# Performance work log

Measured on AMD Instinct MI355X. Metric: run time of the kernel, lower is better.

Reference implementation:

```python
import jax, jax.numpy as jnp
import numpy as np

H = 64          # hidden_size
NG = 5000       # num_genes
B = 32          # num_graphs
N = B * NG      # total nodes
E = 1_600_000   # total edges


def setup_inputs() -> dict:
    key = jax.random.key(0)
    ks = jax.random.split(key, 32)
    def nrm(k, shape, s=0.05):
        return jax.random.normal(k, shape, jnp.float32) * s
    return {
        "x": jax.random.normal(ks[0], (N, 2), jnp.float32),
        "edge_index": jax.random.randint(ks[1], (2, E), 0, N),
        # pert_w: Linear(1, H); gene_basal_w: Linear(1, H)
        "pert_w_W": nrm(ks[2], (H, 1)), "pert_w_b": nrm(ks[3], (H,)),
        "basal_W": nrm(ks[4], (H, 1)), "basal_b": nrm(ks[5], (H,)),
        # gene embedding table (max_norm=True -> rows renormed to norm<=1)
        "emb_table": nrm(ks[6], (NG, H), 0.5),
        # emb_trans: Linear(2H, H)
        "emb_trans_W": nrm(ks[7], (H, 2 * H)), "emb_trans_b": nrm(ks[8], (H,)),
        # pert_base_trans_w: Linear(2H, H)  (gene_pert_agg == 'concat+w')
        "pbt_W": nrm(ks[9], (H, 2 * H)), "pbt_b": nrm(ks[10], (H,)),
        # two GCNConv(H, H) layers
        "gcn1_W": nrm(ks[11], (H, H)), "gcn1_b": nrm(ks[12], (H,)),
        "gcn2_W": nrm(ks[13], (H, H)), "gcn2_b": nrm(ks[14], (H,)),
        # recovery_w: MLP([H, 2H, H, 1]) with BN on first two hidden layers
        "rec_W1": nrm(ks[15], (2 * H, H)), "rec_b1": nrm(ks[16], (2 * H,)),
        "rec_g1": jnp.ones((2 * H,), jnp.float32), "rec_be1": jnp.zeros((2 * H,), jnp.float32),
        "rec_W2": nrm(ks[17], (H, 2 * H)), "rec_b2": nrm(ks[18], (H,)),
        "rec_g2": jnp.ones((H,), jnp.float32), "rec_be2": jnp.zeros((H,), jnp.float32),
        "rec_W3": nrm(ks[19], (1, H)), "rec_b3": nrm(ks[20], (1,)),
    }


def _gcn_conv(h, src, dst, norm, W, b, n_nodes):
    # PyG GCNConv: x' = scatter_add(norm * (x W^T)[src] -> dst) + b, self-loops included in src/dst
    m = h @ W.T                                   # [N, H]
    out = jax.ops.segment_sum(m[src] * norm[:, None], dst, num_segments=n_nodes)
    return out + b


def _batchnorm(z, g, b, eps=1e-5):
    mu = z.mean(0)
    var = z.var(0)
    return (z - mu) * jax.lax.rsqrt(var + eps) * g + b


def reference(x, edge_index, pert_w_W, pert_w_b, basal_W, basal_b, emb_table,
              emb_trans_W, emb_trans_b, pbt_W, pbt_b, gcn1_W, gcn1_b,
              gcn2_W, gcn2_b, rec_W1, rec_b1, rec_g1, rec_be1,
              rec_W2, rec_b2, rec_g2, rec_be2, rec_W3, rec_b3):
    n_nodes = x.shape[0]
    ng = emb_table.shape[0]
    nb = n_nodes // ng

    # GCN normalization with self-loops (computed once, shared by both layers)
    loop = jnp.arange(n_nodes)
    src = jnp.concatenate([edge_index[0], loop])
    dst = jnp.concatenate([edge_index[1], loop])
    deg = jax.ops.segment_sum(jnp.ones_like(src, jnp.float32), dst, num_segments=n_nodes)
    dinv = jnp.where(deg > 0, jax.lax.rsqrt(jnp.maximum(deg, 1.0)), 0.0)
    norm = dinv[src] * dinv[dst]

    pert_emb = x[:, 1:2] @ pert_w_W.T + pert_w_b          # [N, H]
    base = x[:, 0:1] @ basal_W.T + basal_b                # [N, H]

    # nn.Embedding(max_norm=True): renorm rows to max L2 norm of 1
    nrm = jnp.linalg.norm(emb_table, axis=1, keepdims=True)
    emb_n = emb_table * jnp.minimum(1.0, 1.0 / jnp.maximum(nrm, 1e-7))
    emb = jnp.tile(emb_n, (nb, 1))                        # arange(NG).repeat(B) lookup
    base_emb = jnp.concatenate([emb, base], axis=1) @ emb_trans_W.T + emb_trans_b

    def pbt(p, b_):
        return jnp.concatenate([p, b_], axis=1) @ pbt_W.T + pbt_b

    h = pbt(pert_emb, base_emb)
    h = pbt(jax.nn.relu(_gcn_conv(h, src, dst, norm, gcn1_W, gcn1_b, n_nodes)), base_emb)
    h = pbt(jax.nn.relu(_gcn_conv(h, src, dst, norm, gcn2_W, gcn2_b, n_nodes)), base_emb)

    # recovery_w: Linear -> BN -> ReLU -> Linear -> BN -> ReLU -> Linear
    z = jax.nn.relu(_batchnorm(h @ rec_W1.T + rec_b1, rec_g1, rec_be1))
    z = jax.nn.relu(_batchnorm(z @ rec_W2.T + rec_b2, rec_g2, rec_be2))
    out = z @ rec_W3.T + rec_b3                           # [N, 1]
    return out.reshape(nb, ng)
```

## Files before the change

### kernel.cpp

```cpp
#include <hip/hip_runtime.h>


#define GS_GRID 2048
#define GS_BLK  256

enum { A1_=0, A0_=64, C1_=128, C0_=192, D1_=256, D0_=320,
       S1_=384, Q1_=512, SC1_=640, SH1_=768,
       S2_=896, Q2_=960, SC2_=1024, SH2_=1088,
       GD1_=1152, GA1_=1216, G00_=1280,
       GD2_=1344, G02_=1408, RD1_=1472, RD0_=1600, CST_FLOATS=2048 };

__device__ __forceinline__ float wave_sum64(float v) {
#pragma unroll
  for (int o = 32; o; o >>= 1) v += __shfl_xor(v, o, 64);
  return v;
}

__device__ __forceinline__ int rfl(int v) { return __builtin_amdgcn_readfirstlane(v); }

__device__ __forceinline__ float rlane(float v, int k) {
  return __int_as_float(__builtin_amdgcn_readlane(__float_as_int(v), k));
}

__global__ __launch_bounds__(256) void hist_k(const int* __restrict__ ei,
                                              int* __restrict__ hist, int E) {
  __shared__ int h[256];
  const int t = threadIdx.x;
  h[t] = 0;
  __syncthreads();
  const int per = (E + gridDim.x - 1) / gridDim.x;
  const int beg = blockIdx.x * per, end = min(E, beg + per);
  for (int i = beg + t; i < end; i += 256)
    atomicAdd(&h[ei[E + i] >> 10], 1);
  __syncthreads();
  hist[blockIdx.x * 256 + t] = h[t];
}

__global__ void scan1b_k(int* __restrict__ hist, int* __restrict__ bsum) {
  __shared__ int sc[256];
  const int t = threadIdx.x;
  const int b = blockIdx.x;
  int v = hist[t * 256 + b];
  sc[t] = v; __syncthreads();
  for (int o = 1; o < 256; o <<= 1) {
    int x = sc[t]; if (t >= o) x += sc[t - o];
    __syncthreads(); sc[t] = x; __syncthreads();
  }
  hist[t * 256 + b] = sc[t] - v;
  if (t == 255) bsum[b] = sc[t];
}

__global__ void scan2b_k(const int* __restrict__ bsum, int* __restrict__ bucketBase,
                         int* __restrict__ rowptrN, int E) {
  __shared__ int sc[256];
  const int t = threadIdx.x;
  int v = bsum[t];
  sc[t] = v; __syncthreads();
  for (int o = 1; o < 256; o <<= 1) {
    int x = sc[t]; if (t >= o) x += sc[t - o];
    __syncthreads(); sc[t] = x; __syncthreads();
  }
  bucketBase[t] = sc[t] - v;
  if (t == 255) { bucketBase[256] = sc[t]; rowptrN[0] = E; }
}

__global__ __launch_bounds__(256) void bucket_k(const int* __restrict__ ei,
                                                const int* __restrict__ hist,
                                                const int* __restrict__ bucketBase,
                                                int2* __restrict__ eb, int E) {
  __shared__ int cur[256];
  const int t = threadIdx.x;
  cur[t] = hist[blockIdx.x * 256 + t] + bucketBase[t];
  __syncthreads();
  const int per = (E + gridDim.x - 1) / gridDim.x;
  const int beg = blockIdx.x * per, end = min(E, beg + per);
  for (int i = beg + t; i < end; i += 256) {
    int s = ei[i], d = ei[E + i];
    int pos = atomicAdd(&cur[d >> 10], 1);
    eb[pos] = make_int2(s, d);
  }
}

__global__ __launch_bounds__(256) void csr_k(const int2* __restrict__ eb,
                                             const int* __restrict__ bucketBase,
                                             int* __restrict__ rowptr, float* __restrict__ dinv,
                                             int* __restrict__ col, int N) {
  __shared__ int cnt[1024];
  __shared__ int base[1024];
  __shared__ int red[256];
  const int t = threadIdx.x;
  const int k = blockIdx.x;
  const int nodeBeg = k << 10;
  const int segBeg = bucketBase[k], segEnd = bucketBase[k + 1];
#pragma unroll
  for (int j = t; j < 1024; j += 256) cnt[j] = 0;
  __syncthreads();
  for (int i = segBeg + t; i < segEnd; i += 256)
    atomicAdd(&cnt[eb[i].y & 1023], 1);
  __syncthreads();
  int c0 = cnt[4 * t], c1 = cnt[4 * t + 1], c2 = cnt[4 * t + 2], c3 = cnt[4 * t + 3];
  int ts = c0 + c1 + c2 + c3;
  red[t] = ts; __syncthreads();
  for (int o = 1; o < 256; o <<= 1) {
    int x = red[t]; if (t >= o) x += red[t - o];
    __syncthreads(); red[t] = x; __syncthreads();
  }
  int off = red[t] - ts;
  base[4 * t] = off;
  base[4 * t + 1] = off + c0;
  base[4 * t + 2] = off + c0 + c1;
  base[4 * t + 3] = off + c0 + c1 + c2;
#pragma unroll
  for (int u = 0; u < 4; ++u) {
    int j = 4 * t + u;
    int node = nodeBeg + j;
    if (node < N) {
      rowptr[node] = segBeg + base[j];
      dinv[node] = rsqrtf((float)(cnt[j] + 1));
    }
  }
  __syncthreads();
  cnt[4 * t] = base[4 * t]; cnt[4 * t + 1] = base[4 * t + 1];
  cnt[4 * t + 2] = base[4 * t + 2]; cnt[4 * t + 3] = base[4 * t + 3];
  __syncthreads();
  for (int i = segBeg + t; i < segEnd; i += 256) {
    int2 e = eb[i];
    int pos = atomicAdd(&cnt[e.y & 1023], 1);
    col[segBeg + pos] = e.x;
  }
}

__global__ void consts1_k(const float* __restrict__ pbtW, const float* __restrict__ pertW,
                          const float* __restrict__ pertB, const float* __restrict__ etW,
                          const float* __restrict__ basW, const float* __restrict__ basB,
                          const float* __restrict__ etB, float* __restrict__ cst) {
  int h = threadIdx.x;
  float a1 = 0, a0 = 0, c1 = 0, c0 = 0;
  for (int k = 0; k < 64; ++k) {
    float wp = pbtW[h * 128 + k];
    a1 = fmaf(wp, pertW[k], a1);
    a0 = fmaf(wp, pertB[k], a0);
    float we = etW[h * 128 + 64 + k];
    c1 = fmaf(we, basW[k], c1);
    c0 = fmaf(we, basB[k], c0);
  }
  cst[A1_ + h] = a1; cst[A0_ + h] = a0; cst[C1_ + h] = c1; cst[C0_ + h] = c0 + etB[h];
}

__global__ void consts2_k(const float* __restrict__ pbtW, const float* __restrict__ pbtB,
                          float* __restrict__ cst) {
  int h = threadIdx.x;
  float d1 = 0, d0 = 0;
  for (int k = 0; k < 64; ++k) {
    float w = pbtW[h * 128 + 64 + k];
    d1 = fmaf(w, cst[C1_ + k], d1);
    d0 = fmaf(w, cst[C0_ + k], d0);
  }
  cst[D1_ + h] = d1; cst[D0_ + h] = d0 + pbtB[h];
}

__global__ void consts3_k(const float* __restrict__ g1W, float* __restrict__ cst) {
  int h = threadIdx.x;
  float gd1 = 0, ga1 = 0, g00 = 0;
  for (int k = 0; k < 64; ++k) {
    float w = g1W[h * 64 + k];
    gd1 = fmaf(w, cst[D1_ + k], gd1);
    ga1 = fmaf(w, cst[A1_ + k], ga1);
    g00 = fmaf(w, cst[D0_ + k] + cst[A0_ + k], g00);
  }
  cst[GD1_ + h] = gd1; cst[GA1_ + h] = ga1; cst[G00_ + h] = g00;
}

__global__ void consts5_k(const float* __restrict__ g2W, float* __restrict__ cst) {
  int h = threadIdx.x;
  float a = 0, b = 0;
  for (int k = 0; k < 64; ++k) {
    float w = g2W[h * 64 + k];
    a = fmaf(w, cst[D1_ + k], a);
    b = fmaf(w, cst[D0_ + k], b);
  }
  cst[GD2_ + h] = a; cst[G02_ + h] = b;
}

__global__ void consts6_k(const float* __restrict__ rW1, const float* __restrict__ rb1,
                          float* __restrict__ cst) {
  int c = threadIdx.x;
  float a = 0, b = 0;
  for (int k = 0; k < 64; ++k) {
    float w = rW1[c * 64 + k];
    a = fmaf(w, cst[D1_ + k], a);
    b = fmaf(w, cst[D0_ + k], b);
  }
  cst[RD1_ + c] = a; cst[RD0_ + c] = b + rb1[c];
}

__global__ void constsW_k(const float* __restrict__ g2W, const float* __restrict__ rW1,
                          const float* __restrict__ pbtW,
                          float* __restrict__ Wf, float* __restrict__ Wr) {
  const int t = threadIdx.x;
  for (int e = t; e < 4096; e += 256) {
    int c = e >> 6, j = e & 63;
    float s = 0.f;
    for (int h = 0; h < 64; ++h) s = fmaf(g2W[c * 64 + h], pbtW[h * 128 + j], s);
    Wf[e] = s;
  }
  for (int e = t; e < 8192; e += 256) {
    int c = e >> 6, j = e & 63;
    float s = 0.f;
    for (int h = 0; h < 64; ++h) s = fmaf(rW1[c * 64 + h], pbtW[h * 128 + j], s);
    Wr[e] = s;
  }
}

template <bool NORM>
__global__ __launch_bounds__(256) void geneT_k(const float* __restrict__ in,
                                               const float* __restrict__ W, int ldw,
                                               float* __restrict__ out, int NG) {
  const int lane = threadIdx.x & 63;
  const int wid = blockIdx.x * 4 + (threadIdx.x >> 6);
  const int nw = gridDim.x * 4;
  float w[64];
#pragma unroll
  for (int j = 0; j < 16; ++j) {
    float4 v = *reinterpret_cast<const float4*>(W + lane * ldw + 4 * j);
    w[4 * j] = v.x; w[4 * j + 1] = v.y; w[4 * j + 2] = v.z; w[4 * j + 3] = v.w;
  }
  for (int g = wid; g < NG; g += nw) {
    float e = in[g * 64 + lane];
    if (NORM) {
      float sq = wave_sum64(e * e);
      float nrm = sqrtf(sq);
      float s = nrm > 1.f ? 1.f / nrm : 1.f;
      e *= s;
    }
    float acc = 0.f;
#pragma unroll
    for (int k = 0; k < 64; ++k) acc = fmaf(w[k], rlane(e, k), acc);
    out[g * 64 + lane] = acc;
  }
}

__global__ __launch_bounds__(256) void m1_k(const float* __restrict__ x,
                                            const float* __restrict__ embTm1,
                                            const float* __restrict__ dinv,
                                            const float* __restrict__ cst,
                                            float* __restrict__ m1, int N, int NG) {
  int total = N * 16;
  for (int idx = blockIdx.x * blockDim.x + threadIdx.x; idx < total;
       idx += gridDim.x * blockDim.x) {
    int n = idx >> 4, q = idx & 15;
    int g = n % NG;
    float x0 = x[2 * n], x1 = x[2 * n + 1], dn = dinv[n];
    float4 em = *reinterpret_cast<const float4*>(embTm1 + g * 64 + q * 4);
    float4 gd1 = *reinterpret_cast<const float4*>(cst + GD1_ + q * 4);
    float4 ga1 = *reinterpret_cast<const float4*>(cst + GA1_ + q * 4);
    float4 g00 = *reinterpret_cast<const float4*>(cst + G00_ + q * 4);
    float4 mv;
    mv.x = dn * (fmaf(x0, gd1.x, fmaf(x1, ga1.x, em.x + g00.x)));
    mv.y = dn * (fmaf(x0, gd1.y, fmaf(x1, ga1.y, em.y + g00.y)));
    mv.z = dn * (fmaf(x0, gd1.z, fmaf(x1, ga1.z, em.z + g00.z)));
    mv.w = dn * (fmaf(x0, gd1.w, fmaf(x1, ga1.w, em.w + g00.w)));
    reinterpret_cast<float4*>(m1)[idx] = mv;
  }
}

#define XS_STRIDE 130
#define WS_STRIDE 68
#define OS_STRIDE 68
#define OS_WORDS  (128 * OS_STRIDE)
#define WS_WORDS  (64 * WS_STRIDE)
#define LDS_WORDS (OS_WORDS + WS_WORDS + 128)

__device__ __forceinline__ int osslot(int f, int row) { return (f + 2 * row) % 17; }
__device__ __forceinline__ int xswz(int k) { return 2 * ((k >> 2) & 7); }

__device__ __forceinline__ void stage_xsw(const float* __restrict__ in, int ldin,
                                          int inOff, int base, int N, float* Xs, int t) {
#pragma unroll
  for (int c = 0; c < 8; ++c) {
    int lin = c * 256 + t;
    int nl = lin >> 4, k4 = lin & 15;
    int row = base + nl; if (row >= N) row = N - 1;
    float4 v = *reinterpret_cast<const float4*>(in + (size_t)row * ldin + inOff + 4 * k4);
    const int csw = nl ^ (2 * (k4 & 7));
    Xs[(4 * k4 + 0) * XS_STRIDE + csw] = v.x;
    Xs[(4 * k4 + 1) * XS_STRIDE + csw] = v.y;
    Xs[(4 * k4 + 2) * XS_STRIDE + csw] = v.z;
    Xs[(4 * k4 + 3) * XS_STRIDE + csw] = v.w;
  }
}

template <bool MUL_D>
__global__ __launch_bounds__(256, 4) void gemmt_gv_k(
    const float* __restrict__ in,
    const float* __restrict__ W,
    const float* __restrict__ tbl,
    const float* __restrict__ cA, const float* __restrict__ cB,
    const float* __restrict__ x, const float* __restrict__ dinv,
    float* __restrict__ out, int ldout, int N, int NG) {
  __shared__ float lds[LDS_WORDS];
  float* Xs = lds;
  float* Ws = lds + OS_WORDS;
  const int t = threadIdx.x;
  const int base = blockIdx.x << 7;

#pragma unroll
  for (int c = 0; c < 16; ++c) {
    int lin = c * 256 + t;
    int cw = lin >> 6, kw = lin & 63;
    Ws[kw * WS_STRIDE + cw] = W[cw * 64 + kw];
  }
  stage_xsw(in, 64, 0, base, N, Xs, t);
  __syncthreads();

  const int ng = t & 31;
  const int c0 = (t >> 5) * 8;
  float acc[8][4];
#pragma unroll
  for (int i = 0; i < 8; ++i)
#pragma unroll
    for (int j = 0; j < 4; ++j) acc[i][j] = 0.f;
#pragma unroll 4
  for (int k = 0; k < 64; ++k) {
    float4 wa = *reinterpret_cast<const float4*>(Ws + k * WS_STRIDE + c0);
    float4 wb = *reinterpret_cast<const float4*>(Ws + k * WS_STRIDE + c0 + 4);
    const int cb = (2 * ng) ^ xswz(k);
    float2 xa = *reinterpret_cast<const float2*>(Xs + k * XS_STRIDE + cb);
    float2 xb = *reinterpret_cast<const float2*>(Xs + k * XS_STRIDE + cb + 64);
    const float w8[8] = {wa.x, wa.y, wa.z, wa.w, wb.x, wb.y, wb.z, wb.w};
    const float x4[4] = {xa.x, xa.y, xb.x, xb.y};
#pragma unroll
    for (int ci = 0; ci < 8; ++ci)
#pragma unroll
      for (int xi = 0; xi < 4; ++xi)
        acc[ci][xi] = fmaf(w8[ci], x4[xi], acc[ci][xi]);
  }
  __syncthreads();

  const int nd[4] = {2 * ng, 2 * ng + 1, 2 * ng + 64, 2 * ng + 65};
  const int f0 = c0 >> 2;
#pragma unroll
  for (int xi = 0; xi < 4; ++xi) {
    const int r = nd[xi];
    float4 p0 = make_float4(acc[0][xi], acc[1][xi], acc[2][xi], acc[3][xi]);
    float4 p1 = make_float4(acc[4][xi], acc[5][xi], acc[6][xi], acc[7][xi]);
    *reinterpret_cast<float4*>(Xs + r * OS_STRIDE + 4 * osslot(f0, r)) = p0;
    *reinterpret_cast<float4*>(Xs + r * OS_STRIDE + 4 * osslot(f0 + 1, r)) = p1;
  }
  __syncthreads();

  const int q = t & 15;
  const float4 a4 = *reinterpret_cast<const float4*>(cA + 4 * q);
  const float4 b4 = *reinterpret_cast<const float4*>(cB + 4 * q);
#pragma unroll
  for (int c = 0; c < 8; ++c) {
    int nl = c * 16 + (t >> 4);
    int n = base + nl;
    if (n < N) {
      float4 o = *reinterpret_cast<const float4*>(Xs + nl * OS_STRIDE + 4 * osslot(q, nl));
      int g = n % NG;
      float4 tg = *reinterpret_cast<const float4*>(tbl + (size_t)g * 64 + 4 * q);
      float x0 = x[2 * n];
      o.x += fmaf(x0, a4.x, tg.x + b4.x);
      o.y += fmaf(x0, a4.y, tg.y + b4.y);
      o.z += fmaf(x0, a4.z, tg.z + b4.z);
      o.w += fmaf(x0, a4.w, tg.w + b4.w);
      if (MUL_D) {
        float dv = dinv[n];
        o.x *= dv; o.y *= dv; o.z *= dv; o.w *= dv;
      }
      *reinterpret_cast<float4*>(out + (size_t)n * ldout + 4 * q) = o;
    }
  }
}

__global__ __launch_bounds__(256, 4) void gemmt_rec1_k(
    const float* __restrict__ in,
    const float* __restrict__ Wr,
    const float* __restrict__ tblA, const float* __restrict__ tblB,
    const float* __restrict__ cA, const float* __restrict__ cB,
    const float* __restrict__ x,
    float* __restrict__ Z,
    float* __restrict__ sums, float* __restrict__ sqs, int N, int NG) {
  __shared__ float lds[LDS_WORDS];
  float* Xs = lds;
  float* Ws = lds + OS_WORDS;
  float* sred = lds + OS_WORDS + WS_WORDS;
  const int t = threadIdx.x;
  const int base = blockIdx.x << 7;
  if (t < 128) sred[t] = 0.f;

#pragma unroll
  for (int c = 0; c < 16; ++c) {
    int lin = c * 256 + t;
    int cw = lin >> 6, kw = lin & 63;
    Ws[kw * WS_STRIDE + cw] = Wr[cw * 64 + kw];
  }
  stage_xsw(in, 64, 0, base, N, Xs, t);
  __syncthreads();

  const int ng = t & 31;
  const int c0 = (t >> 5) * 8;
  float accA[8][4], accB[8][4];
#pragma unroll
  for (int i = 0; i < 8; ++i)
#pragma unroll
    for (int j = 0; j < 4; ++j) { accA[i][j] = 0.f; accB[i][j] = 0.f; }

#pragma unroll 4
  for (int k = 0; k < 64; ++k) {
    float4 wa = *reinterpret_cast<const float4*>(Ws + k * WS_STRIDE + c0);
    float4 wb = *reinterpret_cast<const float4*>(Ws + k * WS_STRIDE + c0 + 4);
    const int cb = (2 * ng) ^ xswz(k);
    float2 xa = *reinterpret_cast<const float2*>(Xs + k * XS_STRIDE + cb);
    float2 xb = *reinterpret_cast<const float2*>(Xs + k * XS_STRIDE + cb + 64);
    const float w8[8] = {wa.x, wa.y, wa.z, wa.w, wb.x, wb.y, wb.z, wb.w};
    const float x4[4] = {xa.x, xa.y, xb.x, xb.y};
#pragma unroll
    for (int ci = 0; ci < 8; ++ci)
#pragma unroll
      for (int xi = 0; xi < 4; ++xi)
        accA[ci][xi] = fmaf(w8[ci], x4[xi], accA[ci][xi]);
  }
  __syncthreads();
#pragma unroll
  for (int c = 0; c < 16; ++c) {
    int lin = c * 256 + t;
    int cw = lin >> 6, kw = lin & 63;
    Ws[kw * WS_STRIDE + cw] = Wr[(64 + cw) * 64 + kw];
  }
  __syncthreads();
#pragma unroll 4
  for (int k = 0; k < 64; ++k) {
    float4 wa = *reinterpret_cast<const float4*>(Ws + k * WS_STRIDE + c0);
    float4 wb = *reinterpret_cast<const float4*>(Ws + k * WS_STRIDE + c0 + 4);
    const int cb = (2 * ng) ^ xswz(k);
    float2 xa = *reinterpret_cast<const float2*>(Xs + k * XS_STRIDE + cb);
    float2 xb = *reinterpret_cast<const float2*>(Xs + k * XS_STRIDE + cb + 64);
    const float w8[8] = {wa.x, wa.y, wa.z, wa.w, wb.x, wb.y, wb.z, wb.w};
    const float x4[4] = {xa.x, xa.y, xb.x, xb.y};
#pragma unroll
    for (int ci = 0; ci < 8; ++ci)
#pragma unroll
      for (int xi = 0; xi < 4; ++xi)
        accB[ci][xi] = fmaf(w8[ci], x4[xi], accB[ci][xi]);
  }
  __syncthreads();

  const int nd[4] = {2 * ng, 2 * ng + 1, 2 * ng + 64, 2 * ng + 65};
  const int f0 = c0 >> 2;
  const int q = t & 15;

#pragma unroll
  for (int xi = 0; xi < 4; ++xi) {
    const int r = nd[xi];
    float4 p0 = make_float4(accA[0][xi], accA[1][xi], accA[2][xi], accA[3][xi]);
    float4 p1 = make_float4(accA[4][xi], accA[5][xi], accA[6][xi], accA[7][xi]);
    *reinterpret_cast<float4*>(Xs + r * OS_STRIDE + 4 * osslot(f0, r)) = p0;
    *reinterpret_cast<float4*>(Xs + r * OS_STRIDE + 4 * osslot(f0 + 1, r)) = p1;
  }
  __syncthreads();
  {
    const float4 a4 = *reinterpret_cast<const float4*>(cA + 4 * q);
    const float4 b4 = *reinterpret_cast<const float4*>(cB + 4 * q);
    float4 s4 = make_float4(0.f, 0.f, 0.f, 0.f);
    float4 q4 = make_float4(0.f, 0.f, 0.f, 0.f);
#pragma unroll
    for (int c = 0; c < 8; ++c) {
      int nl = c * 16 + (t >> 4);
      int n = base + nl;
      if (n < N) {
        float4 o = *reinterpret_cast<const float4*>(Xs + nl * OS_STRIDE + 4 * osslot(q, nl));
        int g = n % NG;
        float4 tg = *reinterpret_cast<const float4*>(tblA + (size_t)g * 64 + 4 * q);
        float x0 = x[2 * n];
        o.x += fmaf(x0, a4.x, tg.x + b4.x);
        o.y += fmaf(x0, a4.y, tg.y + b4.y);
        o.z += fmaf(x0, a4.z, tg.z + b4.z);
        o.w += fmaf(x0, a4.w, tg.w + b4.w);
        *reinterpret_cast<float4*>(Z + (size_t)n * 128 + 4 * q) = o;
        s4.x += o.x; s4.y += o.y; s4.z += o.z; s4.w += o.w;
        q4.x += o.x * o.x; q4.y += o.y * o.y; q4.z += o.z * o.z; q4.w += o.w * o.w;
      }
    }
    atomicAdd(&sred[4 * q + 0], s4.x); atomicAdd(&sred[4 * q + 1], s4.y);
    atomicAdd(&sred[4 * q + 2], s4.z); atomicAdd(&sred[4 * q + 3], s4.w);
    atomicAdd(&sred[64 + 4 * q + 0], q4.x); atomicAdd(&sred[64 + 4 * q + 1], q4.y);
    atomicAdd(&sred[64 + 4 * q + 2], q4.z); atomicAdd(&sred[64 + 4 * q + 3], q4.w);
  }
  __syncthreads();
  if (t < 64) {
    atomicAdd(&sums[t], sred[t]);
    atomicAdd(&sqs[t], sred[64 + t]);
  }
  __syncthreads();
  if (t < 128) sred[t] = 0.f;
  __syncthreads();

#pragma unroll
  for (int xi = 0; xi < 4; ++xi) {
    const int r = nd[xi];
    float4 p0 = make_float4(accB[0][xi], accB[1][xi], accB[2][xi], accB[3][xi]);
    float4 p1 = make_float4(accB[4][xi], accB[5][xi], accB[6][xi], accB[7][xi]);
    *reinterpret_cast<float4*>(Xs + r * OS_STRIDE + 4 * osslot(f0, r)) = p0;
    *reinterpret_cast<float4*>(Xs + r * OS_STRIDE + 4 * osslot(f0 + 1, r)) = p1;
  }
  __syncthreads();
  {
    const float4 a4 = *reinterpret_cast<const float4*>(cA + 64 + 4 * q);
    const float4 b4 = *reinterpret_cast<const float4*>(cB + 64 + 4 * q);
    float4 s4 = make_float4(0.f, 0.f, 0.f, 0.f);
    float4 q4 = make_float4(0.f, 0.f, 0.f, 0.f);
#pragma unroll
    for (int c = 0; c < 8; ++c) {
      int nl = c * 16 + (t >> 4);
      int n = base + nl;
      if (n < N) {
        float4 o = *reinterpret_cast<const float4*>(Xs + nl * OS_STRIDE + 4 * osslot(q, nl));
        int g = n % NG;
        float4 tg = *reinterpret_cast<const float4*>(tblB + (size_t)g * 64 + 4 * q);
        float x0 = x[2 * n];
        o.x += fmaf(x0, a4.x, tg.x + b4.x);
        o.y += fmaf(x0, a4.y, tg.y + b4.y);
        o.z += fmaf(x0, a4.z, tg.z + b4.z);
        o.w += fmaf(x0, a4.w, tg.w + b4.w);
        *reinterpret_cast<float4*>(Z + (size_t)n * 128 + 64 + 4 * q) = o;
        s4.x += o.x; s4.y += o.y; s4.z += o.z; s4.w += o.w;
        q4.x += o.x * o.x; q4.y += o.y * o.y; q4.z += o.z * o.z; q4.w += o.w * o.w;
      }
    }
    atomicAdd(&sred[4 * q + 0], s4.x); atomicAdd(&sred[4 * q + 1], s4.y);
    atomicAdd(&sred[4 * q + 2], s4.z); atomicAdd(&sred[4 * q + 3], s4.w);
    atomicAdd(&sred[64 + 4 * q + 0], q4.x); atomicAdd(&sred[64 + 4 * q + 1], q4.y);
    atomicAdd(&sred[64 + 4 * q + 2], q4.z); atomicAdd(&sred[64 + 4 * q + 3], q4.w);
  }
  __syncthreads();
  if (t < 64) {
    atomicAdd(&sums[64 + t], sred[t]);
    atomicAdd(&sqs[64 + t], sred[64 + t]);
  }
}

__global__ __launch_bounds__(256, 4) void gemmt_rec2_k(
    const float* __restrict__ Z,
    const float* __restrict__ W,
    const float* __restrict__ b,
    const float* __restrict__ bnsc, const float* __restrict__ bnsh,
    float* __restrict__ out,
    float* __restrict__ sums, float* __restrict__ sqs, int N) {
  __shared__ float lds[LDS_WORDS];
  float* Xs = lds;
  float* Ws = lds + OS_WORDS;
  float* sred = lds + OS_WORDS + WS_WORDS;
  const int t = threadIdx.x;
  const int base = blockIdx.x << 7;
  if (t < 128) sred[t] = 0.f;

  const int ng = t & 31;
  const int c0 = (t >> 5) * 8;
  float acc[8][4];
#pragma unroll
  for (int i = 0; i < 8; ++i)
#pragma unroll
    for (int j = 0; j < 4; ++j) acc[i][j] = 0.f;

  for (int half = 0; half < 2; ++half) {
    if (half) __syncthreads();
    const int ko = half * 64;
#pragma unroll
    for (int c = 0; c < 16; ++c) {
      int lin = c * 256 + t;
      int cw = lin >> 6, kw = lin & 63;
      Ws[kw * WS_STRIDE + cw] = W[cw * 128 + ko + kw];
    }
#pragma unroll
    for (int c = 0; c < 8; ++c) {
      int lin = c * 256 + t;
      int nl = lin >> 4, k4 = lin & 15;
      int row = base + nl; if (row >= N) row = N - 1;
      float4 v = *reinterpret_cast<const float4*>(Z + (size_t)row * 128 + ko + 4 * k4);
      float4 sc = *reinterpret_cast<const float4*>(bnsc + ko + 4 * k4);
      float4 sh = *reinterpret_cast<const float4*>(bnsh + ko + 4 * k4);
      v.x = fmaxf(fmaf(v.x, sc.x, sh.x), 0.f);
      v.y = fmaxf(fmaf(v.y, sc.y, sh.y), 0.f);
      v.z = fmaxf(fmaf(v.z, sc.z, sh.z), 0.f);
      v.w = fmaxf(fmaf(v.w, sc.w, sh.w), 0.f);
      const int csw = nl ^ (2 * (k4 & 7));
      Xs[(4 * k4 + 0) * XS_STRIDE + csw] = v.x;
      Xs[(4 * k4 + 1) * XS_STRIDE + csw] = v.y;
      Xs[(4 * k4 + 2) * XS_STRIDE + csw] = v.z;
      Xs[(4 * k4 + 3) * XS_STRIDE + csw] = v.w;
    }
    __syncthreads();
#pragma unroll 4
    for (int k = 0; k < 64; ++k) {
      float4 wa = *reinterpret_cast<const float4*>(Ws + k * WS_STRIDE + c0);
      float4 wb = *reinterpret_cast<const float4*>(Ws + k * WS_STRIDE + c0 + 4);
      const int cb = (2 * ng) ^ xswz(k);
      float2 xa = *reinterpret_cast<const float2*>(Xs + k * XS_STRIDE + cb);
      float2 xb = *reinterpret_cast<const float2*>(Xs + k * XS_STRIDE + cb + 64);
      const float w8[8] = {wa.x, wa.y, wa.z, wa.w, wb.x, wb.y, wb.z, wb.w};
      const float x4[4] = {xa.x, xa.y, xb.x, xb.y};
#pragma unroll
      for (int ci = 0; ci < 8; ++ci)
#pragma unroll
        for (int xi = 0; xi < 4; ++xi)
          acc[ci][xi] = fmaf(w8[ci], x4[xi], acc[ci][xi]);
    }
  }
  __syncthreads();

  const int nd[4] = {2 * ng, 2 * ng + 1, 2 * ng + 64, 2 * ng + 65};
  const int f0 = c0 >> 2;
#pragma unroll
  for (int xi = 0; xi < 4; ++xi) {
    const int r = nd[xi];
    float4 p0 = make_float4(acc[0][xi], acc[1][xi], acc[2][xi], acc[3][xi]);
    float4 p1 = make_float4(acc[4][xi], acc[5][xi], acc[6][xi], acc[7][xi]);
    *reinterpret_cast<float4*>(Xs + r * OS_STRIDE + 4 * osslot(f0, r)) = p0;
    *reinterpret_cast<float4*>(Xs + r * OS_STRIDE + 4 * osslot(f0 + 1, r)) = p1;
  }
  __syncthreads();

  const int q = t & 15;
  const float4 bb = *reinterpret_cast<const float4*>(b + 4 * q);
  float4 s4 = make_float4(0.f, 0.f, 0.f, 0.f);
  float4 q4 = make_float4(0.f, 0.f, 0.f, 0.f);
#pragma unroll
  for (int c = 0; c < 8; ++c) {
    int nl = c * 16 + (t >> 4);
    int n = base + nl;
    if (n < N) {
      float4 o = *reinterpret_cast<const float4*>(Xs + nl * OS_STRIDE + 4 * osslot(q, nl));
      o.x += bb.x; o.y += bb.y; o.z += bb.z; o.w += bb.w;
      *reinterpret_cast<float4*>(out + (size_t)n * 64 + 4 * q) = o;
      s4.x += o.x; s4.y += o.y; s4.z += o.z; s4.w += o.w;
      q4.x += o.x * o.x; q4.y += o.y * o.y; q4.z += o.z * o.z; q4.w += o.w * o.w;
    }
  }
  atomicAdd(&sred[4 * q + 0], s4.x); atomicAdd(&sred[4 * q + 1], s4.y);
  atomicAdd(&sred[4 * q + 2], s4.z); atomicAdd(&sred[4 * q + 3], s4.w);
  atomicAdd(&sred[64 + 4 * q + 0], q4.x); atomicAdd(&sred[64 + 4 * q + 1], q4.y);
  atomicAdd(&sred[64 + 4 * q + 2], q4.z); atomicAdd(&sred[64 + 4 * q + 3], q4.w);
  __syncthreads();
  if (t < 64) {
    atomicAdd(&sums[t], sred[t]);
    atomicAdd(&sqs[t], sred[64 + t]);
  }
}

__global__ __launch_bounds__(256) void gather_k(const float* __restrict__ m,
                                                const int* __restrict__ rowptr,
                                                const int* __restrict__ col,
                                                const float* __restrict__ dinv,
                                                const float* __restrict__ bias,
                                                float* __restrict__ out, int N) {
  const int lane = threadIdx.x & 63;
  const int wid = blockIdx.x * 4 + (threadIdx.x >> 6);
  const int nw = gridDim.x * 4;
  const float b = bias[lane];
  for (int n = wid; n < N; n += nw) {
    const int nn = rfl(n);
    const float dn = dinv[nn];
    float a0 = m[(size_t)nn * 64 + lane];
    float a1 = 0.f, a2 = 0.f, a3 = 0.f;
    const int beg = rfl(rowptr[nn]), end = rfl(rowptr[nn + 1]);
    for (int base = beg; base < end; base += 64) {
      const int rem = end - base;
      const int kk = rem < 64 ? rem : 64;
      int cv = (lane < kk) ? col[base + lane] : 0;
      int k = 0;
      for (; k + 7 < kk; k += 8) {
        int i0 = __shfl(cv, k, 64),     i1 = __shfl(cv, k + 1, 64);
        int i2 = __shfl(cv, k + 2, 64), i3 = __shfl(cv, k + 3, 64);
        int i4 = __shfl(cv, k + 4, 64), i5 = __shfl(cv, k + 5, 64);
        int i6 = __shfl(cv, k + 6, 64), i7 = __shfl(cv, k + 7, 64);
        float v0 = m[(size_t)i0 * 64 + lane];
        float v1 = m[(size_t)i1 * 64 + lane];
        float v2 = m[(size_t)i2 * 64 + lane];
        float v3 = m[(size_t)i3 * 64 + lane];
        float v4 = m[(size_t)i4 * 64 + lane];
        float v5 = m[(size_t)i5 * 64 + lane];
        float v6 = m[(size_t)i6 * 64 + lane];
        float v7 = m[(size_t)i7 * 64 + lane];
        a0 += v0 + v4; a1 += v1 + v5; a2 += v2 + v6; a3 += v3 + v7;
      }
      for (; k + 1 < kk; k += 2) {
        int i0 = __shfl(cv, k, 64), i1 = __shfl(cv, k + 1, 64);
        float v0 = m[(size_t)i0 * 64 + lane];
        float v1 = m[(size_t)i1 * 64 + lane];
        a0 += v0; a1 += v1;
      }
      if (k < kk) a0 += m[(size_t)__shfl(cv, k, 64) * 64 + lane];
    }
    float acc = (a0 + a1) + (a2 + a3);
    out[(size_t)nn * 64 + lane] = fmaxf(fmaf(dn, acc, b), 0.f);
  }
}

__global__ void bnparam_k(const float* __restrict__ sums, const float* __restrict__ sqs,
                          const float* __restrict__ g, const float* __restrict__ be,
                          float* __restrict__ scale, float* __restrict__ shift, int C,
                          float invN) {
  int t = threadIdx.x;
  if (t < C) {
    float mu = sums[t] * invN;
    float var = fmaxf(sqs[t] * invN - mu * mu, 0.f);
    float sc = g[t] * rsqrtf(var + 1e-5f);
    scale[t] = sc;
    shift[t] = be[t] - mu * sc;
  }
}

__global__ __launch_bounds__(256) void rec3_k(const float* __restrict__ z2,
                                              const float* __restrict__ scale,
                                              const float* __restrict__ shift,
                                              const float* __restrict__ W3,
                                              const float* __restrict__ b3,
                                              float* __restrict__ out, int N) {
  const int lane = threadIdx.x & 63;
  const int wid = blockIdx.x * 4 + (threadIdx.x >> 6);
  const int nw = gridDim.x * 4;
  const float sc = scale[lane], sh = shift[lane], w = W3[lane], b = b3[0];
  for (int n = wid; n < N; n += nw) {
    float v = z2[(size_t)n * 64 + lane];
    v = fmaxf(fmaf(v, sc, sh), 0.f) * w;
    v = wave_sum64(v);
    if (lane == 0) out[n] = v + b;
  }
}

extern "C" void kernel_launch(void* const* d_in, const int* in_sizes, int n_in,
                              void* d_out, int out_size, void* d_ws, size_t ws_size,
                              hipStream_t stream) {
  const float* x     = (const float*)d_in[0];
  const int*   ei    = (const int*)d_in[1];
  const float* pertW = (const float*)d_in[2];
  const float* pertB = (const float*)d_in[3];
  const float* basW  = (const float*)d_in[4];
  const float* basB  = (const float*)d_in[5];
  const float* embTb = (const float*)d_in[6];
  const float* etW   = (const float*)d_in[7];
  const float* etB   = (const float*)d_in[8];
  const float* pbtW  = (const float*)d_in[9];
  const float* pbtB  = (const float*)d_in[10];
  const float* g1W   = (const float*)d_in[11];
  const float* g1B   = (const float*)d_in[12];
  const float* g2W   = (const float*)d_in[13];
  const float* g2B   = (const float*)d_in[14];
  const float* rW1   = (const float*)d_in[15];
  const float* rb1   = (const float*)d_in[16];
  const float* rg1   = (const float*)d_in[17];
  const float* rbe1  = (const float*)d_in[18];
  const float* rW2   = (const float*)d_in[19];
  const float* rb2   = (const float*)d_in[20];
  const float* rg2   = (const float*)d_in[21];
  const float* rbe2  = (const float*)d_in[22];
  const float* rW3   = (const float*)d_in[23];
  const float* rb3   = (const float*)d_in[24];
  float* outp = (float*)d_out;

  const int N  = in_sizes[0] / 2;
  const int E  = in_sizes[1] / 2;
  const int NG = in_sizes[6] / 64;
  const int NB = (N + 1023) >> 10;
  const int NT = (N + 127) >> 7;

  char* p = (char*)d_ws;
  float* cst    = (float*)p; p += CST_FLOATS * 4;
  int*   hist   = (int*)p;   p += 256 * 256 * 4;
  int*   bb     = (int*)p;   p += 1024;
  int*   bsum   = (int*)p;   p += 1024;
  int*   rowptr = (int*)p;   p += (size_t)(N + 64) * 4;
  float* dinv   = (float*)p; p += (size_t)N * 4;
  int*   col    = (int*)p;   p += (size_t)E * 4;
  float* Wf     = (float*)p; p += 4096 * 4;
  float* Wr     = (float*)p; p += 8192 * 4;
  float* embT   = (float*)p; p += (size_t)NG * 64 * 4;
  float* embT2  = (float*)p; p += (size_t)NG * 64 * 4;
  float* embT2g2= (float*)p; p += (size_t)NG * 64 * 4;
  float* embT2rA= (float*)p; p += (size_t)NG * 64 * 4;
  float* embT2rB= (float*)p; p += (size_t)NG * 64 * 4;
  float* z2buf  = (float*)p; p += (size_t)N * 64 * 4;
  float* hb     = (float*)p; p += (size_t)N * 64 * 4;
  float* tmp1   = (float*)p; p += (size_t)N * 64 * 4;
  float* tmp2   = (float*)p; p += (size_t)N * 64 * 4;
  float* Z = hb;
  float* z2 = z2buf;
  float* embTm1 = embT;
  int2*  eb = (int2*)tmp2;

  dim3 blk(GS_BLK), grid(GS_GRID);

  hipMemsetAsync(cst, 0, CST_FLOATS * 4, stream);

  hist_k<<<256, 256, 0, stream>>>(ei, hist, E);
  scan1b_k<<<256, 256, 0, stream>>>(hist, bsum);
  scan2b_k<<<1, 256, 0, stream>>>(bsum, bb, rowptr + N, E);
  bucket_k<<<256, 256, 0, stream>>>(ei, hist, bb, eb, E);
  csr_k<<<NB, 256, 0, stream>>>(eb, bb, rowptr, dinv, col, N);

  consts1_k<<<1, 64, 0, stream>>>(pbtW, pertW, pertB, etW, basW, basB, etB, cst);
  consts2_k<<<1, 64, 0, stream>>>(pbtW, pbtB, cst);
  consts3_k<<<1, 64, 0, stream>>>(g1W, cst);
  consts5_k<<<1, 64, 0, stream>>>(g2W, cst);
  consts6_k<<<1, 128, 0, stream>>>(rW1, rb1, cst);
  constsW_k<<<1, 256, 0, stream>>>(g2W, rW1, pbtW, Wf, Wr);
  geneT_k<true><<<256, 256, 0, stream>>>(embTb, etW, 128, embT, NG);
  geneT_k<false><<<256, 256, 0, stream>>>(embT, pbtW + 64, 128, embT2, NG);
  geneT_k<false><<<256, 256, 0, stream>>>(embT2, g1W, 64, embTm1, NG);
  geneT_k<false><<<256, 256, 0, stream>>>(embT2, g2W, 64, embT2g2, NG);
  geneT_k<false><<<256, 256, 0, stream>>>(embT2, rW1, 64, embT2rA, NG);
  geneT_k<false><<<256, 256, 0, stream>>>(embT2, rW1 + 64 * 64, 64, embT2rB, NG);
  m1_k<<<grid, blk, 0, stream>>>(x, embTm1, dinv, cst, tmp1, N, NG);

  gather_k<<<grid, blk, 0, stream>>>(tmp1, rowptr, col, dinv, g1B, tmp2, N);
  gemmt_gv_k<true><<<NT, blk, 0, stream>>>(
      tmp2, Wf, embT2g2, cst + GD2_, cst + G02_, x, dinv, tmp1, 64, N, NG);
  gather_k<<<grid, blk, 0, stream>>>(tmp1, rowptr, col, dinv, g2B, tmp2, N);

  gemmt_rec1_k<<<NT, blk, 0, stream>>>(
      tmp2, Wr, embT2rA, embT2rB, cst + RD1_, cst + RD0_, x, Z,
      cst + S1_, cst + Q1_, N, NG);
  bnparam_k<<<1, 128, 0, stream>>>(cst + S1_, cst + Q1_, rg1, rbe1,
                                   cst + SC1_, cst + SH1_, 128, 1.0f / (float)N);
  gemmt_rec2_k<<<NT, blk, 0, stream>>>(Z, rW2, rb2, cst + SC1_, cst + SH1_,
                                       z2, cst + S2_, cst + Q2_, N);
  bnparam_k<<<1, 64, 0, stream>>>(cst + S2_, cst + Q2_, rg2, rbe2,
                                  cst + SC2_, cst + SH2_, 64, 1.0f / (float)N);
  rec3_k<<<grid, blk, 0, stream>>>(z2, cst + SC2_, cst + SH2_, rW3, rb3, outp, N);
}
```

Baseline: 489.0 us.

## Fuse first-layer message construction into the gather via compact node records

Instead of materializing the full N×64 first-layer message tensor and then gathering it, a small per-node record (x0, x1, dinv, gene id) is written and the gather recomputes each neighbor's message on the fly from the gene embedding table and the constants. This removes a large write and a large scattered read of 64-float rows, replacing them with 16-byte record reads plus reads from a small, cache-resident 5000×64 table. The cost is more per-edge arithmetic and a dependent load chain (record, then table) per neighbor. The gather also applies bias and relu, matching what the old gather did.

After: 489.0 us. No clear change (-0.0%).

```diff
diff --git a/kernel.cpp b/kernel.cpp
--- a/kernel.cpp
+++ b/kernel.cpp
@@ -240,27 +240,62 @@
   }
 }
 
-__global__ __launch_bounds__(256) void m1_k(const float* __restrict__ x,
-                                            const float* __restrict__ embTm1,
-                                            const float* __restrict__ dinv,
-                                            const float* __restrict__ cst,
-                                            float* __restrict__ m1, int N, int NG) {
-  int total = N * 16;
-  for (int idx = blockIdx.x * blockDim.x + threadIdx.x; idx < total;
-       idx += gridDim.x * blockDim.x) {
-    int n = idx >> 4, q = idx & 15;
+__global__ __launch_bounds__(256) void nrec_k(const float* __restrict__ x,
+                                              const float* __restrict__ dinv,
+                                              float4* __restrict__ nrec, int N, int NG) {
+  for (int n = blockIdx.x * blockDim.x + threadIdx.x; n < N; n += gridDim.x * blockDim.x) {
     int g = n % NG;
-    float x0 = x[2 * n], x1 = x[2 * n + 1], dn = dinv[n];
-    float4 em = *reinterpret_cast<const float4*>(embTm1 + g * 64 + q * 4);
-    float4 gd1 = *reinterpret_cast<const float4*>(cst + GD1_ + q * 4);
-    float4 ga1 = *reinterpret_cast<const float4*>(cst + GA1_ + q * 4);
-    float4 g00 = *reinterpret_cast<const float4*>(cst + G00_ + q * 4);
-    float4 mv;
-    mv.x = dn * (fmaf(x0, gd1.x, fmaf(x1, ga1.x, em.x + g00.x)));
-    mv.y = dn * (fmaf(x0, gd1.y, fmaf(x1, ga1.y, em.y + g00.y)));
-    mv.z = dn * (fmaf(x0, gd1.z, fmaf(x1, ga1.z, em.z + g00.z)));
-    mv.w = dn * (fmaf(x0, gd1.w, fmaf(x1, ga1.w, em.w + g00.w)));
-    reinterpret_cast<float4*>(m1)[idx] = mv;
+    nrec[n] = make_float4(x[2 * n], x[2 * n + 1], dinv[n], __int_as_float(g));
+  }
+}
+
+__global__ __launch_bounds__(256) void gather1_k(
+    const float4* __restrict__ nrec, const float* __restrict__ embTm1,
+    const int* __restrict__ rowptr, const int* __restrict__ col,
+    const float* __restrict__ dinv, const float* __restrict__ cst,
+    const float* __restrict__ bias, float* __restrict__ out, int N) {
+  const int lane = threadIdx.x & 63;
+  const int wid = blockIdx.x * 4 + (threadIdx.x >> 6);
+  const int nw = gridDim.x * 4;
+  const float gd1 = cst[GD1_ + lane];
+  const float ga1 = cst[GA1_ + lane];
+  const float g00 = cst[G00_ + lane];
+  const float b = bias[lane];
+  for (int n = wid; n < N; n += nw) {
+    const int nn = rfl(n);
+    const float dn = dinv[nn];
+    float4 r0 = nrec[nn];
+    float e0 = embTm1[(size_t)__float_as_int(r0.w) * 64 + lane];
+    float a0 = r0.z * fmaf(r0.x, gd1, fmaf(r0.y, ga1, e0 + g00));
+    float a1 = 0.f, a2 = 0.f, a3 = 0.f;
+    const int beg = rfl(rowptr[nn]), end = rfl(rowptr[nn + 1]);
+    for (int base = beg; base < end; base += 64) {
+      const int rem = end - base;
+      const int kk = rem < 64 ? rem : 64;
+      int cv = (lane < kk) ? col[base + lane] : 0;
+      int k = 0;
+      for (; k + 3 < kk; k += 4) {
+        int s0 = __shfl(cv, k, 64),     s1 = __shfl(cv, k + 1, 64);
+        int s2 = __shfl(cv, k + 2, 64), s3 = __shfl(cv, k + 3, 64);
+        float4 q0 = nrec[s0], q1 = nrec[s1], q2 = nrec[s2], q3 = nrec[s3];
+        float v0 = embTm1[(size_t)__float_as_int(q0.w) * 64 + lane];
+        float v1 = embTm1[(size_t)__float_as_int(q1.w) * 64 + lane];
+        float v2 = embTm1[(size_t)__float_as_int(q2.w) * 64 + lane];
+        float v3 = embTm1[(size_t)__float_as_int(q3.w) * 64 + lane];
+        a0 += q0.z * fmaf(q0.x, gd1, fmaf(q0.y, ga1, v0 + g00));
+        a1 += q1.z * fmaf(q1.x, gd1, fmaf(q1.y, ga1, v1 + g00));
+        a2 += q2.z * fmaf(q2.x, gd1, fmaf(q2.y, ga1, v2 + g00));
+        a3 += q3.z * fmaf(q3.x, gd1, fmaf(q3.y, ga1, v3 + g00));
+      }
+      for (; k < kk; ++k) {
+        int s0 = __shfl(cv, k, 64);
+        float4 q0 = nrec[s0];
+        float v0 = embTm1[(size_t)__float_as_int(q0.w) * 64 + lane];
+        a0 += q0.z * fmaf(q0.x, gd1, fmaf(q0.y, ga1, v0 + g00));
+      }
+    }
+    float acc = (a0 + a1) + (a2 + a3);
+    out[(size_t)nn * 64 + lane] = fmaxf(fmaf(dn, acc, b), 0.f);
   }
 }
 
@@ -789,6 +824,7 @@
   float* z2 = z2buf;
   float* embTm1 = embT;
   int2*  eb = (int2*)tmp2;
+  float4* nrec = (float4*)tmp1;
 
   dim3 blk(GS_BLK), grid(GS_GRID);
 
@@ -812,9 +848,10 @@
   geneT_k<false><<<256, 256, 0, stream>>>(embT2, g2W, 64, embT2g2, NG);
   geneT_k<false><<<256, 256, 0, stream>>>(embT2, rW1, 64, embT2rA, NG);
   geneT_k<false><<<256, 256, 0, stream>>>(embT2, rW1 + 64 * 64, 64, embT2rB, NG);
-  m1_k<<<grid, blk, 0, stream>>>(x, embTm1, dinv, cst, tmp1, N, NG);
-
-  gather_k<<<grid, blk, 0, stream>>>(tmp1, rowptr, col, dinv, g1B, tmp2, N);
+  nrec_k<<<grid, blk, 0, stream>>>(x, dinv, nrec, N, NG);
+
+  gather1_k<<<grid, blk, 0, stream>>>(nrec, embTm1, rowptr, col, dinv, cst,
+                                      g1B, tmp2, N);
   gemmt_gv_k<true><<<NT, blk, 0, stream>>>(
       tmp2, Wf, embT2g2, cst + GD2_, cst + G02_, x, dinv, tmp1, 64, N, NG);
   gather_k<<<grid, blk, 0, stream>>>(tmp1, rowptr, col, dinv, g2B, tmp2, N);
```
